# Optimization experiments

Hardware: AMD Instinct MI355X
Metric: run time of the kernel (lower is better)

Reference implementation:

```python
import jax, jax.numpy as jnp
import numpy as np

B, N, DIM, H = 4, 2048, 1024, 8
HD = DIM // H
SCALE = HD ** -0.5


def setup_inputs() -> dict:
    key = jax.random.key(0)
    ks = jax.random.split(key, 9)
    inp = {
        "q": jax.random.normal(ks[0], (B, N, DIM), dtype=jnp.float32),
        "k": jax.random.normal(ks[1], (B, N, DIM), dtype=jnp.float32),
        "v": jax.random.normal(ks[2], (B, N, DIM), dtype=jnp.float32),
        "trans_mat": jax.random.normal(ks[3], (B, N, N), dtype=jnp.float32),
        # torch Linear weights: [out_features, in_features]; qkv_bias=False
        "Wq": jax.random.normal(ks[4], (DIM, DIM), dtype=jnp.float32) * (DIM ** -0.5),
        "Wk": jax.random.normal(ks[5], (DIM, DIM), dtype=jnp.float32) * (DIM ** -0.5),
        "Wv": jax.random.normal(ks[6], (DIM, DIM), dtype=jnp.float32) * (DIM ** -0.5),
        "Wp": jax.random.normal(ks[7], (DIM, DIM), dtype=jnp.float32) * (DIM ** -0.5),
        "bp": jax.random.normal(ks[8], (DIM,), dtype=jnp.float32) * 0.01,
    }
    return inp


def reference(q, k, v, trans_mat, Wq, Wk, Wv, Wp, bp):
    Bq, Nq, C = q.shape
    # project and split heads: [B, H, N, HD]
    qh = (q @ Wq.T).reshape(Bq, Nq, H, HD).transpose(0, 2, 1, 3)
    kh = (k @ Wk.T).reshape(Bq, -1, H, HD).transpose(0, 2, 1, 3)
    vh = (v @ Wv.T).reshape(Bq, -1, H, HD).transpose(0, 2, 1, 3)
    # scaled scores gated elementwise by trans_mat (broadcast over heads)
    scores = jnp.einsum("bhqd,bhkd->bhqk", qh, kh) * SCALE
    gated = scores * trans_mat[:, None, :, :]
    # softmax over full row, then zero out positions where gated == 0
    sm = jax.nn.softmax(gated, axis=-1)
    attn = jnp.where(gated != 0, sm, jnp.zeros((), dtype=sm.dtype))
    x = jnp.einsum("bhqk,bhkd->bhqd", attn, vh)
    x = x.transpose(0, 2, 1, 3).reshape(Bq, Nq, C)
    return x @ Wp.T + bp
```

## Files before the change

### kernel.cpp

```cpp
#include <hip/hip_runtime.h>
#include <hip/hip_bf16.h>
#include <stdint.h>

#define B_    4
#define N_    2048
#define DIM_  1024
#define H_    8
#define HD_   128
#define MTOK  (B_ * N_)
#define SCALE_  0.08838834764831845f
#define LOG2E_  1.4426950408889634f
#define QSCALE_ (SCALE_ * LOG2E_)

typedef unsigned short u16;
typedef __attribute__((ext_vector_type(4))) float f32x4;
typedef __attribute__((ext_vector_type(8))) short s16x8;
typedef __attribute__((ext_vector_type(8))) u16  u16x8;
typedef __attribute__((ext_vector_type(4))) u16  u16x4;

__device__ __forceinline__ u16 f2bf(float f) {
    uint32_t i = __builtin_bit_cast(uint32_t, f);
    return (u16)((i + 0x7FFFu + ((i >> 16) & 1u)) >> 16);
}

__device__ __forceinline__ void gl_lds16(const u16* g, u16* l) {
    __builtin_amdgcn_global_load_lds((const __attribute__((address_space(1))) void*)g,
                                     (__attribute__((address_space(3))) void*)l,
                                     16, 0, 0);
}

__global__ __launch_bounds__(256) void cvt_f32_bf16(const float* __restrict__ src,
                                                    u16* __restrict__ dst, int n) {
    int i = (blockIdx.x * 256 + threadIdx.x) * 4;
    int stride = gridDim.x * 256 * 4;
    for (; i < n; i += stride) {
        float4 v = *(const float4*)(src + i);
        u16x4 o;
        o.x = f2bf(v.x); o.y = f2bf(v.y); o.z = f2bf(v.z); o.w = f2bf(v.w);
        *(u16x4*)(dst + i) = o;
    }
}

template <int MODE>
__global__ __launch_bounds__(256) void gemm_bt(const u16* __restrict__ A,
                                               const u16* __restrict__ Bt,
                                               void* __restrict__ Cout,
                                               const float* __restrict__ bias,
                                               float scale, int M, int NN, int K) {
    __shared__ __align__(16) u16 lga[128 * 64];
    __shared__ __align__(16) u16 lgb[128 * 64];
    const int tid  = threadIdx.x;
    const int lane = tid & 63, wave = tid >> 6;
    const int wm = wave >> 1, wn = wave & 1;
    const int row0 = blockIdx.y * 128, col0 = blockIdx.x * 128;

    f32x4 acc[4][4] = {};

    auto stageLds = [&](const u16* G, u16* L, int rowbase, int k0) {
        #pragma unroll
        for (int i = 0; i < 4; i++) {
            int rb = wave * 32 + i * 8;
            int r  = rb + (lane >> 3);
            int cc = (lane & 7) ^ (lane >> 3);
            gl_lds16(G + (size_t)(rowbase + r) * K + k0 + cc * 8, L + rb * 64);
        }
    };

    for (int k0 = 0; k0 < K; k0 += 64) {
        stageLds(A,  lga, row0, k0);
        stageLds(Bt, lgb, col0, k0);
        __syncthreads();
        #pragma unroll
        for (int kk = 0; kk < 2; kk++) {
            s16x8 af[4], bfr[4];
            #pragma unroll
            for (int mi = 0; mi < 4; mi++) {
                int r = wm * 64 + mi * 16 + (lane & 15);
                int sc = (kk * 4 + (lane >> 4)) ^ (lane & 7);
                af[mi] = *(const s16x8*)(&lga[r * 64 + sc * 8]);
            }
            #pragma unroll
            for (int ni = 0; ni < 4; ni++) {
                int r = wn * 64 + ni * 16 + (lane & 15);
                int sc = (kk * 4 + (lane >> 4)) ^ (lane & 7);
                bfr[ni] = *(const s16x8*)(&lgb[r * 64 + sc * 8]);
            }
            #pragma unroll
            for (int mi = 0; mi < 4; mi++)
                #pragma unroll
                for (int ni = 0; ni < 4; ni++)
                    acc[mi][ni] = __builtin_amdgcn_mfma_f32_16x16x32_bf16(
                        af[mi], bfr[ni], acc[mi][ni], 0, 0, 0);
        }
        __syncthreads();
    }

    #pragma unroll
    for (int mi = 0; mi < 4; mi++) {
        #pragma unroll
        for (int ni = 0; ni < 4; ni++) {
            #pragma unroll
            for (int r = 0; r < 4; r++) {
                int grow = row0 + wm * 64 + mi * 16 + ((lane >> 4) << 2) + r;
                int gcol = col0 + wn * 64 + ni * 16 + (lane & 15);
                float vv = acc[mi][ni][r];
                if (MODE == 2) {
                    ((float*)Cout)[(size_t)grow * NN + gcol] = vv + bias[gcol];
                } else {
                    vv *= scale;
                    int bb = grow >> 11, n = grow & (N_ - 1);
                    int hh = gcol >> 7,  d = gcol & (HD_ - 1);
                    size_t idx = (MODE == 0)
                        ? ((size_t)(bb * H_ + hh) * N_ + n) * HD_ + d
                        : ((size_t)(bb * H_ + hh) * HD_ + d) * N_ + n;
                    ((u16*)Cout)[idx] = f2bf(vv);
                }
            }
        }
    }
}

__global__ __launch_bounds__(512) void attn_kernel(const u16* __restrict__ Qh,
                                                   const u16* __restrict__ Kh,
                                                   const u16* __restrict__ Vt,
                                                   const float* __restrict__ trans,
                                                   u16* __restrict__ xout) {
    __shared__ __align__(16) u16 kt[64 * 128];
    __shared__ __align__(16) u16 vt[128 * 64];
    __shared__ __align__(16) u16 plds[8][16 * 72];

    const int tid = threadIdx.x, lane = tid & 63, wave = tid >> 6;
    const int qt = blockIdx.x, h = blockIdx.y, b = blockIdx.z;
    const int qrow_base = qt * 128 + wave * 16;

    const u16* Qbh = Qh + (size_t)(b * H_ + h) * N_ * HD_;
    const u16* Kbh = Kh + (size_t)(b * H_ + h) * N_ * HD_;
    const u16* Vbh = Vt + (size_t)(b * H_ + h) * HD_ * N_;
    const float* trow = trans + (size_t)b * N_ * N_
                      + (size_t)(qrow_base + ((lane >> 4) << 2)) * N_ + (lane & 15);

    s16x8 qf[4];
    {
        int r = qrow_base + (lane & 15);
        #pragma unroll
        for (int kd = 0; kd < 4; kd++)
            qf[kd] = *(const s16x8*)(Qbh + (size_t)r * HD_ + kd * 32 + ((lane >> 4) << 3));
    }

    auto stageKV = [&](int kv0) {
        int rbk = wave * 8, rbv = wave * 16;
        #pragma unroll
        for (int j = 0; j < 2; j++) {
            int c = j * 64 + lane;
            int rk = rbk + (c >> 4);
            int ck = (c & 15) ^ (rk & 15);
            gl_lds16(Kbh + (size_t)(kv0 + rk) * HD_ + ck * 8, kt + rbk * 128 + j * 512);
            int rv = rbv + (c >> 3);
            int cv = (c & 7) ^ (rv & 7);
            gl_lds16(Vbh + (size_t)rv * N_ + kv0 + cv * 8, vt + rbv * 64 + j * 512);
        }
    };

    float m[4], l[4];
    #pragma unroll
    for (int r = 0; r < 4; r++) { m[r] = -3.0e38f; l[r] = 0.f; }
    f32x4 ao[8] = {};

    for (int kv0 = 0; kv0 < N_; kv0 += 64) {
        stageKV(kv0);
        __syncthreads();

        f32x4 s[4] = {};
        #pragma unroll
        for (int kd = 0; kd < 4; kd++)
            #pragma unroll
            for (int ni = 0; ni < 4; ni++) {
                int r = ni * 16 + (lane & 15);
                int sc = (kd * 4 + (lane >> 4)) ^ (lane & 15);
                s16x8 bfr = *(const s16x8*)(&kt[r * 128 + sc * 8]);
                s[ni] = __builtin_amdgcn_mfma_f32_16x16x32_bf16(qf[kd], bfr, s[ni], 0, 0, 0);
            }

        float pmax[4] = {-3.0e38f, -3.0e38f, -3.0e38f, -3.0e38f};
        #pragma unroll
        for (int ni = 0; ni < 4; ni++)
            #pragma unroll
            for (int r = 0; r < 4; r++) {
                float tt = trow[(size_t)r * N_ + kv0 + ni * 16];
                float gg = s[ni][r] * tt;
                s[ni][r] = gg;
                pmax[r] = fmaxf(pmax[r], gg);
            }
        #pragma unroll
        for (int r = 0; r < 4; r++) {
            float p = pmax[r];
            p = fmaxf(p, __shfl_xor(p, 1));
            p = fmaxf(p, __shfl_xor(p, 2));
            p = fmaxf(p, __shfl_xor(p, 4));
            p = fmaxf(p, __shfl_xor(p, 8));
            pmax[r] = p;
        }
        bool need = false;
        #pragma unroll
        for (int r = 0; r < 4; r++) need = need || (pmax[r] > m[r] + 8.0f);
        if (__any(need)) {
            #pragma unroll
            for (int r = 0; r < 4; r++) {
                float mn = fmaxf(m[r], pmax[r]);
                float sfv = __builtin_amdgcn_exp2f(m[r] - mn);
                m[r] = mn;
                l[r] *= sfv;
                #pragma unroll
                for (int t = 0; t < 8; t++) ao[t][r] *= sfv;
            }
        }
        float rowsum[4] = {0.f, 0.f, 0.f, 0.f};
        u16* pw = &plds[wave][0];
        #pragma unroll
        for (int ni = 0; ni < 4; ni++)
            #pragma unroll
            for (int r = 0; r < 4; r++) {
                float gg = s[ni][r];
                float e = __builtin_amdgcn_exp2f(gg - m[r]);
                rowsum[r] += e;
                float pe = (gg != 0.0f) ? e : 0.0f;
                pw[(((lane >> 4) << 2) + r) * 72 + ni * 16 + (lane & 15)] = f2bf(pe);
            }
        #pragma unroll
        for (int r = 0; r < 4; r++) {
            float ssum = rowsum[r];
            ssum += __shfl_xor(ssum, 1);
            ssum += __shfl_xor(ssum, 2);
            ssum += __shfl_xor(ssum, 4);
            ssum += __shfl_xor(ssum, 8);
            l[r] += ssum;
        }
        #pragma unroll
        for (int kk = 0; kk < 2; kk++) {
            s16x8 pa = *(const s16x8*)(&pw[(lane & 15) * 72 + kk * 32 + ((lane >> 4) << 3)]);
            #pragma unroll
            for (int t = 0; t < 8; t++) {
                int r = t * 16 + (lane & 15);
                int sc = (kk * 4 + (lane >> 4)) ^ (lane & 7);
                s16x8 vb = *(const s16x8*)(&vt[r * 64 + sc * 8]);
                ao[t] = __builtin_amdgcn_mfma_f32_16x16x32_bf16(pa, vb, ao[t], 0, 0, 0);
            }
        }
        __syncthreads();
    }

    #pragma unroll
    for (int r = 0; r < 4; r++) {
        float inv = 1.0f / l[r];
        int n = qrow_base + ((lane >> 4) << 2) + r;
        u16* orow = xout + ((size_t)(b * N_ + n)) * DIM_ + h * HD_;
        #pragma unroll
        for (int t = 0; t < 8; t++)
            orow[t * 16 + (lane & 15)] = f2bf(ao[t][r] * inv);
    }
}

extern "C" void kernel_launch(void* const* d_in, const int* in_sizes, int n_in,
                              void* d_out, int out_size, void* d_ws, size_t ws_size,
                              hipStream_t stream) {
    const float* q     = (const float*)d_in[0];
    const float* k     = (const float*)d_in[1];
    const float* v     = (const float*)d_in[2];
    const float* trans = (const float*)d_in[3];
    const float* Wq    = (const float*)d_in[4];
    const float* Wk    = (const float*)d_in[5];
    const float* Wv    = (const float*)d_in[6];
    const float* Wp    = (const float*)d_in[7];
    const float* bp    = (const float*)d_in[8];

    char* ws = (char*)d_ws;
    u16* tmp = (u16*)(ws);
    u16* wqb = (u16*)(ws + (16u << 20));
    u16* wkb = (u16*)(ws + (18u << 20));
    u16* wvb = (u16*)(ws + (20u << 20));
    u16* wpb = (u16*)(ws + (22u << 20));
    u16* QhB = (u16*)(ws + (24u << 20));
    u16* KhB = (u16*)(ws + (40u << 20));
    u16* VtB = (u16*)(ws + (56u << 20));
    u16* xb  = tmp;

    dim3 blk(256);
    cvt_f32_bf16<<<dim3(1024), blk, 0, stream>>>(Wq, wqb, DIM_ * DIM_);
    cvt_f32_bf16<<<dim3(1024), blk, 0, stream>>>(Wk, wkb, DIM_ * DIM_);
    cvt_f32_bf16<<<dim3(1024), blk, 0, stream>>>(Wv, wvb, DIM_ * DIM_);
    cvt_f32_bf16<<<dim3(1024), blk, 0, stream>>>(Wp, wpb, DIM_ * DIM_);

    dim3 pg(DIM_ / 128, MTOK / 128);

    cvt_f32_bf16<<<dim3(8192), blk, 0, stream>>>(q, tmp, MTOK * DIM_);
    gemm_bt<0><<<pg, blk, 0, stream>>>(tmp, wqb, QhB, nullptr, QSCALE_, MTOK, DIM_, DIM_);
    cvt_f32_bf16<<<dim3(8192), blk, 0, stream>>>(k, tmp, MTOK * DIM_);
    gemm_bt<0><<<pg, blk, 0, stream>>>(tmp, wkb, KhB, nullptr, 1.0f, MTOK, DIM_, DIM_);
    cvt_f32_bf16<<<dim3(8192), blk, 0, stream>>>(v, tmp, MTOK * DIM_);
    gemm_bt<1><<<pg, blk, 0, stream>>>(tmp, wvb, VtB, nullptr, 1.0f, MTOK, DIM_, DIM_);

    attn_kernel<<<dim3(N_ / 128, H_, B_), dim3(512), 0, stream>>>(QhB, KhB, VtB, trans, xb);

    gemm_bt<2><<<pg, blk, 0, stream>>>(xb, wpb, d_out, bp, 1.0f, MTOK, DIM_, DIM_);
}
```

Measured before the change: 289.8 us.

## Fuse input bf16 conversion into GEMMs and double-buffer a larger-tile attention kernel

The separate f32-to-bf16 conversion passes over q/k/v are removed; the projection GEMMs now load fp32 A tiles and convert them into LDS using packed bf16 conversion. The four weight conversions are merged into one launch. The attention kernel now handles 32 query rows per wave (256 per block), reusing each K/V LDS fragment for two MFMAs. It double-buffers K/V tiles so the next tile loads during compute, prefetches the trans_mat values before the QK MFMAs, remaps blocks to a different order, and raises wave priority around MFMA sections. These changes cut extra global memory traffic and kernel launches, at the cost of higher register and LDS pressure, a grid half as large, and a synchronous fp32 A load path in the GEMM.

```diff
diff --git a/kernel.cpp b/kernel.cpp
--- a/kernel.cpp
+++ b/kernel.cpp
@@ -13,36 +13,43 @@
 #define QSCALE_ (SCALE_ * LOG2E_)
 
 typedef unsigned short u16;
-typedef __attribute__((ext_vector_type(4))) float f32x4;
-typedef __attribute__((ext_vector_type(8))) short s16x8;
-typedef __attribute__((ext_vector_type(8))) u16  u16x8;
-typedef __attribute__((ext_vector_type(4))) u16  u16x4;
+typedef __attribute__((ext_vector_type(4)))  float f32x4;
+typedef __attribute__((ext_vector_type(8)))  short s16x8;
+typedef __attribute__((ext_vector_type(8)))  u16  u16x8;
+typedef __attribute__((ext_vector_type(4)))  u16  u16x4;
+typedef __attribute__((ext_vector_type(4)))  unsigned u32x4;
 
 __device__ __forceinline__ u16 f2bf(float f) {
     uint32_t i = __builtin_bit_cast(uint32_t, f);
     return (u16)((i + 0x7FFFu + ((i >> 16) & 1u)) >> 16);
 }
-
+__device__ __forceinline__ unsigned pk_bf16(float a, float b) {
+    unsigned r;
+    asm("v_cvt_pk_bf16_f32 %0, %1, %2" : "=v"(r) : "v"(a), "v"(b));
+    return r;
+}
 __device__ __forceinline__ void gl_lds16(const u16* g, u16* l) {
     __builtin_amdgcn_global_load_lds((const __attribute__((address_space(1))) void*)g,
                                      (__attribute__((address_space(3))) void*)l,
                                      16, 0, 0);
 }
 
-__global__ __launch_bounds__(256) void cvt_f32_bf16(const float* __restrict__ src,
-                                                    u16* __restrict__ dst, int n) {
-    int i = (blockIdx.x * 256 + threadIdx.x) * 4;
-    int stride = gridDim.x * 256 * 4;
-    for (; i < n; i += stride) {
-        float4 v = *(const float4*)(src + i);
-        u16x4 o;
-        o.x = f2bf(v.x); o.y = f2bf(v.y); o.z = f2bf(v.z); o.w = f2bf(v.w);
-        *(u16x4*)(dst + i) = o;
-    }
-}
-
-template <int MODE>
-__global__ __launch_bounds__(256) void gemm_bt(const u16* __restrict__ A,
+__global__ __launch_bounds__(256) void cvt_w4(const float* __restrict__ s0,
+                                              const float* __restrict__ s1,
+                                              const float* __restrict__ s2,
+                                              const float* __restrict__ s3,
+                                              u16* __restrict__ dst) {
+    const float* s = blockIdx.y == 0 ? s0 : blockIdx.y == 1 ? s1 : blockIdx.y == 2 ? s2 : s3;
+    u16* d = dst + (size_t)blockIdx.y * (DIM_ * DIM_);
+    int i = (blockIdx.x * 256 + threadIdx.x) * 8;
+    float4 a = *(const float4*)(s + i);
+    float4 b = *(const float4*)(s + i + 4);
+    u32x4 w = {pk_bf16(a.x, a.y), pk_bf16(a.z, a.w), pk_bf16(b.x, b.y), pk_bf16(b.z, b.w)};
+    *(u16x8*)(d + i) = __builtin_bit_cast(u16x8, w);
+}
+
+template <int MODE, bool AF32>
+__global__ __launch_bounds__(256) void gemm_bt(const void* __restrict__ Ain,
                                                const u16* __restrict__ Bt,
                                                void* __restrict__ Cout,
                                                const float* __restrict__ bias,
@@ -53,6 +60,8 @@
     const int lane = tid & 63, wave = tid >> 6;
     const int wm = wave >> 1, wn = wave & 1;
     const int row0 = blockIdx.y * 128, col0 = blockIdx.x * 128;
+    const float* Af = (const float*)Ain;
+    const u16*  Ab  = (const u16*)Ain;
 
     f32x4 acc[4][4] = {};
 
@@ -65,9 +74,23 @@
             gl_lds16(G + (size_t)(rowbase + r) * K + k0 + cc * 8, L + rb * 64);
         }
     };
+    auto stageA32 = [&](int k0) {
+        #pragma unroll
+        for (int i = 0; i < 4; i++) {
+            int p = tid + i * 256, r = p >> 3, pc = p & 7;
+            int sc = pc ^ (r & 7);
+            const float* src = Af + (size_t)(row0 + r) * K + k0 + pc * 8;
+            float4 a = *(const float4*)(src);
+            float4 b = *(const float4*)(src + 4);
+            u32x4 w = {pk_bf16(a.x, a.y), pk_bf16(a.z, a.w),
+                       pk_bf16(b.x, b.y), pk_bf16(b.z, b.w)};
+            *(u16x8*)(&lga[r * 64 + sc * 8]) = __builtin_bit_cast(u16x8, w);
+        }
+    };
 
     for (int k0 = 0; k0 < K; k0 += 64) {
-        stageLds(A,  lga, row0, k0);
+        if (AF32) stageA32(k0);
+        else      stageLds(Ab, lga, row0, k0);
         stageLds(Bt, lgb, col0, k0);
         __syncthreads();
         #pragma unroll
@@ -120,144 +143,190 @@
     }
 }
 
-__global__ __launch_bounds__(512) void attn_kernel(const u16* __restrict__ Qh,
-                                                   const u16* __restrict__ Kh,
-                                                   const u16* __restrict__ Vt,
-                                                   const float* __restrict__ trans,
-                                                   u16* __restrict__ xout) {
-    __shared__ __align__(16) u16 kt[64 * 128];
-    __shared__ __align__(16) u16 vt[128 * 64];
-    __shared__ __align__(16) u16 plds[8][16 * 72];
+__global__ __launch_bounds__(512, 2) void attn_kernel(const u16* __restrict__ Qh,
+                                                      const u16* __restrict__ Kh,
+                                                      const u16* __restrict__ Vt,
+                                                      const float* __restrict__ trans,
+                                                      u16* __restrict__ xout) {
+    __shared__ __align__(16) u16 kt[2][64 * 128];
+    __shared__ __align__(16) u16 vt[2][128 * 64];
+    __shared__ __align__(16) u16 plds[8][32 * 72];
 
     const int tid = threadIdx.x, lane = tid & 63, wave = tid >> 6;
-    const int qt = blockIdx.x, h = blockIdx.y, b = blockIdx.z;
-    const int qrow_base = qt * 128 + wave * 16;
-
-    const u16* Qbh = Qh + (size_t)(b * H_ + h) * N_ * HD_;
-    const u16* Kbh = Kh + (size_t)(b * H_ + h) * N_ * HD_;
-    const u16* Vbh = Vt + (size_t)(b * H_ + h) * HD_ * N_;
-    const float* trow = trans + (size_t)b * N_ * N_
-                      + (size_t)(qrow_base + ((lane >> 4) << 2)) * N_ + (lane & 15);
-
-    s16x8 qf[4];
-    {
-        int r = qrow_base + (lane & 15);
+    const int L = lane & 15, g = lane >> 4;
+
+    int lin  = blockIdx.x + 8 * (blockIdx.y + 8 * blockIdx.z);
+    int nlin = (lin & 7) * 32 + (lin >> 3);
+    const int qt = nlin & 7, hh = (nlin >> 3) & 7, b = nlin >> 6;
+    const int q0 = qt * 256 + wave * 32;
+
+    const u16* Qbh = Qh + (size_t)(b * H_ + hh) * N_ * HD_;
+    const u16* Kbh = Kh + (size_t)(b * H_ + hh) * N_ * HD_;
+    const u16* Vbh = Vt + (size_t)(b * H_ + hh) * HD_ * N_;
+    const float* trb = trans + (size_t)b * N_ * N_;
+
+    s16x8 qf[2][4];
+    #pragma unroll
+    for (int rg = 0; rg < 2; rg++) {
+        int r = q0 + rg * 16 + L;
         #pragma unroll
         for (int kd = 0; kd < 4; kd++)
-            qf[kd] = *(const s16x8*)(Qbh + (size_t)r * HD_ + kd * 32 + ((lane >> 4) << 3));
+            qf[rg][kd] = *(const s16x8*)(Qbh + (size_t)r * HD_ + kd * 32 + g * 8);
     }
 
-    auto stageKV = [&](int kv0) {
+    auto stageKV = [&](int kv0, int bi) {
         int rbk = wave * 8, rbv = wave * 16;
         #pragma unroll
         for (int j = 0; j < 2; j++) {
             int c = j * 64 + lane;
-            int rk = rbk + (c >> 4);
-            int ck = (c & 15) ^ (rk & 15);
-            gl_lds16(Kbh + (size_t)(kv0 + rk) * HD_ + ck * 8, kt + rbk * 128 + j * 512);
-            int rv = rbv + (c >> 3);
-            int cv = (c & 7) ^ (rv & 7);
-            gl_lds16(Vbh + (size_t)rv * N_ + kv0 + cv * 8, vt + rbv * 64 + j * 512);
+            int rk = rbk + (c >> 4), ck = (c & 15) ^ (rk & 15);
+            gl_lds16(Kbh + (size_t)(kv0 + rk) * HD_ + ck * 8, &kt[bi][rbk * 128 + j * 512]);
+            int rv = rbv + (c >> 3), cv = (c & 7) ^ (rv & 7);
+            gl_lds16(Vbh + (size_t)rv * N_ + kv0 + cv * 8, &vt[bi][rbv * 64 + j * 512]);
         }
     };
 
-    float m[4], l[4];
+    float m[2][4], l[2][4];
     #pragma unroll
-    for (int r = 0; r < 4; r++) { m[r] = -3.0e38f; l[r] = 0.f; }
-    f32x4 ao[8] = {};
-
-    for (int kv0 = 0; kv0 < N_; kv0 += 64) {
-        stageKV(kv0);
-        __syncthreads();
-
-        f32x4 s[4] = {};
+    for (int rg = 0; rg < 2; rg++)
+        #pragma unroll
+        for (int r = 0; r < 4; r++) { m[rg][r] = -3.0e38f; l[rg][r] = 0.f; }
+    f32x4 ao[2][8] = {};
+
+    stageKV(0, 0);
+    __syncthreads();
+
+    for (int it = 0; it < N_ / 64; it++) {
+        const int kv0 = it * 64, cur = it & 1;
+        if (it + 1 < N_ / 64) stageKV(kv0 + 64, cur ^ 1);
+
+        float tt[2][4][4];
+        #pragma unroll
+        for (int rg = 0; rg < 2; rg++)
+            #pragma unroll
+            for (int ni = 0; ni < 4; ni++)
+                #pragma unroll
+                for (int r = 0; r < 4; r++)
+                    tt[rg][ni][r] = trb[(size_t)(q0 + rg * 16 + g * 4 + r) * N_
+                                        + kv0 + ni * 16 + L];
+
+        f32x4 s[2][4] = {};
+        __builtin_amdgcn_s_setprio(1);
         #pragma unroll
         for (int kd = 0; kd < 4; kd++)
             #pragma unroll
             for (int ni = 0; ni < 4; ni++) {
-                int r = ni * 16 + (lane & 15);
-                int sc = (kd * 4 + (lane >> 4)) ^ (lane & 15);
-                s16x8 bfr = *(const s16x8*)(&kt[r * 128 + sc * 8]);
-                s[ni] = __builtin_amdgcn_mfma_f32_16x16x32_bf16(qf[kd], bfr, s[ni], 0, 0, 0);
-            }
-
-        float pmax[4] = {-3.0e38f, -3.0e38f, -3.0e38f, -3.0e38f};
-        #pragma unroll
-        for (int ni = 0; ni < 4; ni++)
+                int r = ni * 16 + L;
+                int sc = (kd * 4 + g) ^ (r & 15);
+                s16x8 kf = *(const s16x8*)(&kt[cur][r * 128 + sc * 8]);
+                s[0][ni] = __builtin_amdgcn_mfma_f32_16x16x32_bf16(qf[0][kd], kf, s[0][ni], 0, 0, 0);
+                s[1][ni] = __builtin_amdgcn_mfma_f32_16x16x32_bf16(qf[1][kd], kf, s[1][ni], 0, 0, 0);
+            }
+        __builtin_amdgcn_s_setprio(0);
+
+        float pmax[2][4] = {{-3.0e38f, -3.0e38f, -3.0e38f, -3.0e38f},
+                            {-3.0e38f, -3.0e38f, -3.0e38f, -3.0e38f}};
+        #pragma unroll
+        for (int rg = 0; rg < 2; rg++)
+            #pragma unroll
+            for (int ni = 0; ni < 4; ni++)
+                #pragma unroll
+                for (int r = 0; r < 4; r++) {
+                    float gg = s[rg][ni][r] * tt[rg][ni][r];
+                    s[rg][ni][r] = gg;
+                    pmax[rg][r] = fmaxf(pmax[rg][r], gg);
+                }
+        #pragma unroll
+        for (int rg = 0; rg < 2; rg++)
             #pragma unroll
             for (int r = 0; r < 4; r++) {
-                float tt = trow[(size_t)r * N_ + kv0 + ni * 16];
-                float gg = s[ni][r] * tt;
-                s[ni][r] = gg;
-                pmax[r] = fmaxf(pmax[r], gg);
-            }
-        #pragma unroll
-        for (int r = 0; r < 4; r++) {
-            float p = pmax[r];
-            p = fmaxf(p, __shfl_xor(p, 1));
-            p = fmaxf(p, __shfl_xor(p, 2));
-            p = fmaxf(p, __shfl_xor(p, 4));
-            p = fmaxf(p, __shfl_xor(p, 8));
-            pmax[r] = p;
-        }
+                float p = pmax[rg][r];
+                p = fmaxf(p, __shfl_xor(p, 1));
+                p = fmaxf(p, __shfl_xor(p, 2));
+                p = fmaxf(p, __shfl_xor(p, 4));
+                p = fmaxf(p, __shfl_xor(p, 8));
+                pmax[rg][r] = p;
+            }
         bool need = false;
         #pragma unroll
-        for (int r = 0; r < 4; r++) need = need || (pmax[r] > m[r] + 8.0f);
+        for (int rg = 0; rg < 2; rg++)
+            #pragma unroll
+            for (int r = 0; r < 4; r++) need = need || (pmax[rg][r] > m[rg][r] + 8.0f);
         if (__any(need)) {
             #pragma unroll
+            for (int rg = 0; rg < 2; rg++)
+                #pragma unroll
+                for (int r = 0; r < 4; r++) {
+                    float mn = fmaxf(m[rg][r], pmax[rg][r]);
+                    float sfv = __builtin_amdgcn_exp2f(m[rg][r] - mn);
+                    m[rg][r] = mn;
+                    l[rg][r] *= sfv;
+                    #pragma unroll
+                    for (int t = 0; t < 8; t++) ao[rg][t][r] *= sfv;
+                }
+        }
+
+        float rowsum[2][4] = {};
+        u16* pw = &plds[wave][0];
+        #pragma unroll
+        for (int rg = 0; rg < 2; rg++)
+            #pragma unroll
             for (int r = 0; r < 4; r++) {
-                float mn = fmaxf(m[r], pmax[r]);
-                float sfv = __builtin_amdgcn_exp2f(m[r] - mn);
-                m[r] = mn;
-                l[r] *= sfv;
-                #pragma unroll
-                for (int t = 0; t < 8; t++) ao[t][r] *= sfv;
-            }
-        }
-        float rowsum[4] = {0.f, 0.f, 0.f, 0.f};
-        u16* pw = &plds[wave][0];
-        #pragma unroll
-        for (int ni = 0; ni < 4; ni++)
+                float pe[4];
+                #pragma unroll
+                for (int ni = 0; ni < 4; ni++) {
+                    float gg = s[rg][ni][r];
+                    float e = __builtin_amdgcn_exp2f(gg - m[rg][r]);
+                    rowsum[rg][r] += e;
+                    pe[ni] = (gg != 0.0f) ? e : 0.0f;
+                }
+                unsigned p01 = pk_bf16(pe[0], pe[1]);
+                unsigned p23 = pk_bf16(pe[2], pe[3]);
+                u16* pr = pw + (rg * 16 + g * 4 + r) * 72 + L;
+                pr[0]  = (u16)p01; pr[16] = (u16)(p01 >> 16);
+                pr[32] = (u16)p23; pr[48] = (u16)(p23 >> 16);
+            }
+        #pragma unroll
+        for (int rg = 0; rg < 2; rg++)
             #pragma unroll
             for (int r = 0; r < 4; r++) {
-                float gg = s[ni][r];
-                float e = __builtin_amdgcn_exp2f(gg - m[r]);
-                rowsum[r] += e;
-                float pe = (gg != 0.0f) ? e : 0.0f;
-                pw[(((lane >> 4) << 2) + r) * 72 + ni * 16 + (lane & 15)] = f2bf(pe);
-            }
-        #pragma unroll
-        for (int r = 0; r < 4; r++) {
-            float ssum = rowsum[r];
-            ssum += __shfl_xor(ssum, 1);
-            ssum += __shfl_xor(ssum, 2);
-            ssum += __shfl_xor(ssum, 4);
-            ssum += __shfl_xor(ssum, 8);
-            l[r] += ssum;
-        }
+                float ssum = rowsum[rg][r];
+                ssum += __shfl_xor(ssum, 1);
+                ssum += __shfl_xor(ssum, 2);
+                ssum += __shfl_xor(ssum, 4);
+                ssum += __shfl_xor(ssum, 8);
+                l[rg][r] += ssum;
+            }
+
+        __builtin_amdgcn_s_setprio(1);
         #pragma unroll
         for (int kk = 0; kk < 2; kk++) {
-            s16x8 pa = *(const s16x8*)(&pw[(lane & 15) * 72 + kk * 32 + ((lane >> 4) << 3)]);
+            s16x8 pa0 = *(const s16x8*)(&pw[(L)      * 72 + kk * 32 + g * 8]);
+            s16x8 pa1 = *(const s16x8*)(&pw[(16 + L) * 72 + kk * 32 + g * 8]);
             #pragma unroll
             for (int t = 0; t < 8; t++) {
-                int r = t * 16 + (lane & 15);
-                int sc = (kk * 4 + (lane >> 4)) ^ (lane & 7);
-                s16x8 vb = *(const s16x8*)(&vt[r * 64 + sc * 8]);
-                ao[t] = __builtin_amdgcn_mfma_f32_16x16x32_bf16(pa, vb, ao[t], 0, 0, 0);
-            }
-        }
+                int r = t * 16 + L;
+                int sc = (kk * 4 + g) ^ (r & 7);
+                s16x8 vf = *(const s16x8*)(&vt[cur][r * 64 + sc * 8]);
+                ao[0][t] = __builtin_amdgcn_mfma_f32_16x16x32_bf16(pa0, vf, ao[0][t], 0, 0, 0);
+                ao[1][t] = __builtin_amdgcn_mfma_f32_16x16x32_bf16(pa1, vf, ao[1][t], 0, 0, 0);
+            }
+        }
+        __builtin_amdgcn_s_setprio(0);
         __syncthreads();
     }
 
     #pragma unroll
-    for (int r = 0; r < 4; r++) {
-        float inv = 1.0f / l[r];
-        int n = qrow_base + ((lane >> 4) << 2) + r;
-        u16* orow = xout + ((size_t)(b * N_ + n)) * DIM_ + h * HD_;
-        #pragma unroll
-        for (int t = 0; t < 8; t++)
-            orow[t * 16 + (lane & 15)] = f2bf(ao[t][r] * inv);
-    }
+    for (int rg = 0; rg < 2; rg++)
+        #pragma unroll
+        for (int r = 0; r < 4; r++) {
+            float inv = 1.0f / l[rg][r];
+            int n = q0 + rg * 16 + g * 4 + r;
+            u16* orow = xout + ((size_t)(b * N_ + n)) * DIM_ + hh * HD_;
+            #pragma unroll
+            for (int t = 0; t < 8; t++)
+                orow[t * 16 + L] = f2bf(ao[rg][t][r] * inv);
+        }
 }
 
 extern "C" void kernel_launch(void* const* d_in, const int* in_sizes, int n_in,
@@ -274,7 +343,7 @@
     const float* bp    = (const float*)d_in[8];
 
     char* ws = (char*)d_ws;
-    u16* tmp = (u16*)(ws);
+    u16* xb  = (u16*)(ws);
     u16* wqb = (u16*)(ws + (16u << 20));
     u16* wkb = (u16*)(ws + (18u << 20));
     u16* wvb = (u16*)(ws + (20u << 20));
@@ -282,24 +351,16 @@
     u16* QhB = (u16*)(ws + (24u << 20));
     u16* KhB = (u16*)(ws + (40u << 20));
     u16* VtB = (u16*)(ws + (56u << 20));
-    u16* xb  = tmp;
-
-    dim3 blk(256);
-    cvt_f32_bf16<<<dim3(1024), blk, 0, stream>>>(Wq, wqb, DIM_ * DIM_);
-    cvt_f32_bf16<<<dim3(1024), blk, 0, stream>>>(Wk, wkb, DIM_ * DIM_);
-    cvt_f32_bf16<<<dim3(1024), blk, 0, stream>>>(Wv, wvb, DIM_ * DIM_);
-    cvt_f32_bf16<<<dim3(1024), blk, 0, stream>>>(Wp, wpb, DIM_ * DIM_);
+
+    cvt_w4<<<dim3(512, 4), dim3(256), 0, stream>>>(Wq, Wk, Wv, Wp, wqb);
 
     dim3 pg(DIM_ / 128, MTOK / 128);
 
-    cvt_f32_bf16<<<dim3(8192), blk, 0, stream>>>(q, tmp, MTOK * DIM_);
-    gemm_bt<0><<<pg, blk, 0, stream>>>(tmp, wqb, QhB, nullptr, QSCALE_, MTOK, DIM_, DIM_);
-    cvt_f32_bf16<<<dim3(8192), blk, 0, stream>>>(k, tmp, MTOK * DIM_);
-    gemm_bt<0><<<pg, blk, 0, stream>>>(tmp, wkb, KhB, nullptr, 1.0f, MTOK, DIM_, DIM_);
-    cvt_f32_bf16<<<dim3(8192), blk, 0, stream>>>(v, tmp, MTOK * DIM_);
-    gemm_bt<1><<<pg, blk, 0, stream>>>(tmp, wvb, VtB, nullptr, 1.0f, MTOK, DIM_, DIM_);
-
-    attn_kernel<<<dim3(N_ / 128, H_, B_), dim3(512), 0, stream>>>(QhB, KhB, VtB, trans, xb);
-
-    gemm_bt<2><<<pg, blk, 0, stream>>>(xb, wpb, d_out, bp, 1.0f, MTOK, DIM_, DIM_);
-}
+    gemm_bt<0, true><<<pg, dim3(256), 0, stream>>>(q, wqb, QhB, nullptr, QSCALE_, MTOK, DIM_, DIM_);
+    gemm_bt<0, true><<<pg, dim3(256), 0, stream>>>(k, wkb, KhB, nullptr, 1.0f, MTOK, DIM_, DIM_);
+    gemm_bt<1, true><<<pg, dim3(256), 0, stream>>>(v, wvb, VtB, nullptr, 1.0f, MTOK, DIM_, DIM_);
+
+    attn_kernel<<<dim3(N_ / 256, H_, B_), dim3(512), 0, stream>>>(QhB, KhB, VtB, trans, xb);
+
+    gemm_bt<2, false><<<pg, dim3(256), 0, stream>>>(xb, wpb, d_out, bp, 1.0f, MTOK, DIM_, DIM_);
+}
```

New measurement: 324.0 us. 1.12x slower.
